# Kernel optimization log

Hardware: AMD Instinct MI355X
Metric: run time of the kernel (lower is better)

Reference implementation:

```python
import jax, jax.numpy as jnp
import numpy as np

E = 16        # num_experts
TOPK = 2      # num_experts_per_tok


def setup_inputs() -> dict:
    key = jax.random.key(0)
    ks = jax.random.split(key, 8)
    B, S, H, I, IS = 4, 2048, 1024, 512, 2048
    std = 0.02
    return {
        "hidden_states": jax.random.normal(ks[0], (B, S, H), jnp.float32),
        "gate_w": jax.random.normal(ks[1], (E, H), jnp.float32) * std,
        "gate_up_proj": jax.random.normal(ks[2], (E, 2 * I, H), jnp.float32) * std,
        "down_proj": jax.random.normal(ks[3], (E, H, I), jnp.float32) * std,
        "shared_gate_proj": jax.random.normal(ks[4], (IS, H), jnp.float32) * std,
        "shared_up_proj": jax.random.normal(ks[5], (IS, H), jnp.float32) * std,
        "shared_down_proj": jax.random.normal(ks[6], (H, IS), jnp.float32) * std,
        "shared_expert_gate_w": jax.random.normal(ks[7], (1, H), jnp.float32) * std,
    }


def _moe(x, gate_w, gate_up_proj, down_proj, sgp, sup, sdp, segw):
    # x: [N, H] flattened tokens
    N = x.shape[0]
    router_logits = x @ gate_w.T                      # [N, E]
    probs = jax.nn.softmax(router_logits, axis=-1)
    routing_weights, selected = jax.lax.top_k(probs, TOPK)   # [N, TOPK]
    routing_weights = routing_weights / routing_weights.sum(-1, keepdims=True)
    # combine weights scattered into dense [N, E] (per-token per-expert gate)
    combine = jnp.zeros((N, E), x.dtype).at[jnp.arange(N)[:, None], selected].add(routing_weights)

    def body(acc, ws):
        gu_w, d_w, cw = ws                            # [2I,H], [H,I], [N]
        gu = x @ gu_w.T                               # [N, 2I]
        g, u = jnp.split(gu, 2, axis=-1)
        h = jax.nn.silu(g) * u                        # [N, I]
        return acc + cw[:, None] * (h @ d_w.T), None

    expert_out, _ = jax.lax.scan(body, jnp.zeros_like(x), (gate_up_proj, down_proj, combine.T))

    # shared expert with sigmoid token gate
    shared_h = jax.nn.silu(x @ sgp.T) * (x @ sup.T)   # [N, IS]
    shared_out = (shared_h @ sdp.T) * jax.nn.sigmoid(x @ segw.T)  # [N, H]
    out = expert_out + shared_out

    # aux (load-balancing) loss
    counts = jnp.sum(jax.nn.one_hot(selected, E, dtype=x.dtype), axis=(0, 1))  # [E]
    frac_tokens = counts / (N * TOPK)
    frac_probs = probs.sum(0) / N
    aux_loss = E * jnp.sum(frac_tokens * frac_probs)
    return out, aux_loss


def reference(hidden_states, gate_w, gate_up_proj, down_proj, shared_gate_proj, shared_up_proj, shared_down_proj, shared_expert_gate_w):
    B, S, H = hidden_states.shape
    out, aux = _moe(hidden_states.reshape(-1, H), gate_w, gate_up_proj, down_proj,
                    shared_gate_proj, shared_up_proj, shared_down_proj, shared_expert_gate_w)
    return out.reshape(B, S, H), aux
```

## Files before the change

### kernel.cpp

```cpp
#include <hip/hip_runtime.h>
#include <hip/hip_bf16.h>
#include <stdint.h>


#define N_TOK 8192
#define HDIM 1024
#define NEXP 16
#define IEXP 512
#define ISH 2048

typedef __bf16 bf16x8 __attribute__((ext_vector_type(8)));
typedef float f32x4 __attribute__((ext_vector_type(4)));

#define OFF_XBF   ((size_t)0)
#define OFF_WSG   ((size_t)16777216)
#define OFF_WSU   ((size_t)20971520)
#define OFF_WSD   ((size_t)25165824)
#define OFF_SH    ((size_t)29360128)
#define OFF_HEXP  ((size_t)62914560)
#define OFF_IDS   ((size_t)79691776)
#define OFF_META  ((size_t)80216064)
#define OFF_SIG   ((size_t)80216320)
#define OFF_LG    ((size_t)80249088)
#define OFF_SLOT  ((size_t)81297664)
#define OFF_TWAB  ((size_t)81363200)

#define WGU_NEW     ((size_t)81428736)
#define NEED_MERGED ((size_t)(WGU_NEW + 33554432))

static __device__ __forceinline__ unsigned short f2bf(float f) {
  unsigned int u = __float_as_uint(f);
  u += 0x7fffu + ((u >> 16) & 1u);
  return (unsigned short)(u >> 16);
}
static __device__ __forceinline__ int pack_bf2(float a, float b) {
  return (int)f2bf(a) | ((int)f2bf(b) << 16);
}
static __device__ __forceinline__ float bf2f(unsigned short u) {
  return __uint_as_float(((unsigned int)u) << 16);
}
static __device__ __forceinline__ void gl_lds16(const void* g, void* l) {
  __builtin_amdgcn_global_load_lds(
      (const __attribute__((address_space(1))) unsigned int*)g,
      (__attribute__((address_space(3))) unsigned int*)l, 16, 0, 0);
}
static __device__ __forceinline__ void barf() {
  asm volatile("" ::: "memory");
  __builtin_amdgcn_s_barrier();
  asm volatile("" ::: "memory");
}

__global__ void cvt_kernel(const float* __restrict__ src,
                           unsigned short* __restrict__ dst, int n4) {
  int i = blockIdx.x * 256 + threadIdx.x;
  if (i >= n4) return;
  float4 v = ((const float4*)src)[i];
  uint2 o;
  o.x = (unsigned)pack_bf2(v.x, v.y);
  o.y = (unsigned)pack_bf2(v.z, v.w);
  ((uint2*)dst)[i] = o;
}

__global__ __launch_bounds__(256) void logits_kernel(
    const float* __restrict__ X, const float* __restrict__ GW,
    const float* __restrict__ SEGW, float* __restrict__ LG,
    unsigned short* __restrict__ XBF) {
  int wid = threadIdx.x >> 6, lane = threadIdx.x & 63;
  int tok = blockIdx.x * 4 + wid;
  const float* xr = X + (size_t)tok * HDIM;
  unsigned short* xw = XBF + (size_t)tok * HDIM;
  float xv[16];
#pragma unroll
  for (int i = 0; i < 16; i++) xv[i] = xr[lane + 64 * i];
#pragma unroll
  for (int i = 0; i < 16; i++) xw[lane + 64 * i] = f2bf(xv[i]);
  float myv = 0.f;
#pragma unroll
  for (int e = 0; e < 17; e++) {
    const float* wr = (e < 16) ? (GW + (size_t)e * HDIM) : SEGW;
    float p = 0.f;
#pragma unroll
    for (int i = 0; i < 16; i++) p += xv[i] * wr[lane + 64 * i];
#pragma unroll
    for (int off = 32; off >= 1; off >>= 1) p += __shfl_xor(p, off, 64);
    if (lane == e) myv = p;
  }
  if (lane < 17) LG[(size_t)tok * 32 + lane] = myv;
}

__global__ __launch_bounds__(256) void route_kernel(
    const float* __restrict__ LG, int* __restrict__ cnt,
    float* __restrict__ pps, int* __restrict__ ids,
    int* __restrict__ slotAB, float* __restrict__ twAB,
    float* __restrict__ sig) {
  __shared__ int lcnt[16];
  __shared__ int lbase[16];
  __shared__ float lps[16];
  int tid = threadIdx.x;
  int tok = blockIdx.x * 256 + tid;
  if (tid < 16) { lcnt[tid] = 0; lps[tid] = 0.f; }
  __syncthreads();
  const float4* row = (const float4*)(LG + (size_t)tok * 32);
  float4 v0 = row[0], v1 = row[1], v2 = row[2], v3 = row[3];
  float g16 = row[4].x;
  float lg[16] = {v0.x, v0.y, v0.z, v0.w, v1.x, v1.y, v1.z, v1.w,
                  v2.x, v2.y, v2.z, v2.w, v3.x, v3.y, v3.z, v3.w};
  float mx = lg[0];
#pragma unroll
  for (int e = 1; e < 16; e++) mx = fmaxf(mx, lg[e]);
  float pr[16], s = 0.f;
#pragma unroll
  for (int e = 0; e < 16; e++) { pr[e] = __expf(lg[e] - mx); s += pr[e]; }
  float inv_s = 1.f / s;
  float p1 = -1.f, p2 = -1.f; int i1 = 0, i2 = 0;
#pragma unroll
  for (int e = 0; e < 16; e++) {
    if (pr[e] > p1) { p2 = p1; i2 = i1; p1 = pr[e]; i1 = e; }
    else if (pr[e] > p2) { p2 = pr[e]; i2 = e; }
  }
  float wsum = p1 + p2;
  int s1 = atomicAdd(&lcnt[i1], 1);
  int s2 = atomicAdd(&lcnt[i2], 1);
#pragma unroll
  for (int e = 0; e < 16; e++) atomicAdd(&lps[e], pr[e] * inv_s);
  sig[tok] = 1.f / (1.f + __expf(-g16));
  __syncthreads();
  if (tid < 16) {
    lbase[tid] = atomicAdd(&cnt[tid], lcnt[tid]);
    atomicAdd(&pps[tid], lps[tid]);
  }
  __syncthreads();
  int sl1 = lbase[i1] + s1, sl2 = lbase[i2] + s2;
  ids[i1 * N_TOK + sl1] = tok;
  ids[i2 * N_TOK + sl2] = tok;
  slotAB[tok * 2]     = (i1 << 14) | sl1;
  slotAB[tok * 2 + 1] = (i2 << 14) | sl2;
  twAB[tok * 2]     = p1 / wsum;
  twAB[tok * 2 + 1] = p2 / wsum;
}

__global__ void offs_aux_kernel(const int* __restrict__ cnt, int* __restrict__ off,
                                const float* __restrict__ probs_sum,
                                float* __restrict__ out_aux) {
  if (threadIdx.x == 0 && blockIdx.x == 0) {
    int run = 0; float aux = 0.f;
    for (int e = 0; e < NEXP; e++) {
      off[e] = run; run += cnt[e];
      aux += ((float)cnt[e] / (float)(N_TOK * 2)) * (probs_sum[e] / (float)N_TOK);
    }
    off[16] = run;
    *out_aux = (float)NEXP * aux;
  }
}

template <int TMODE>
__global__ __launch_bounds__(512, 2) void g8p_kernel(
    const unsigned short* __restrict__ A0,
    const unsigned short* __restrict__ Bg,
    const unsigned short* __restrict__ Bu,
    const unsigned short* __restrict__ Bgu,
    const unsigned short* __restrict__ Bd,
    const int* __restrict__ ids, const int* __restrict__ cnt,
    const int* __restrict__ off,
    unsigned short* __restrict__ Osh,
    unsigned short* __restrict__ Ohex,
    unsigned short* __restrict__ Oeout) {
  constexpr int KD = (TMODE == 2) ? IEXP : HDIM;
  constexpr int NK = KD / 64;
  extern __shared__ unsigned short lds[];

  int rmode, e = 0, bx, by, m0step;
  if constexpr (TMODE == 3) {
    int id = blockIdx.x;
    if (id < 512) { rmode = 0; bx = id & 15; by = id >> 4; m0step = 8192; }
    else {
      int id2 = id - 512;
      rmode = 1; e = id2 >> 5; bx = id2 & 3; by = (id2 >> 2) & 7; m0step = 2048;
    }
  } else if constexpr (TMODE == 0) {
    rmode = 0; bx = blockIdx.x; by = blockIdx.y; m0step = 8192;
  } else if constexpr (TMODE == 1) {
    rmode = 1; e = blockIdx.z; bx = blockIdx.x; by = blockIdx.y;
    m0step = (int)gridDim.y * 256;
  } else {
    rmode = 2; e = blockIdx.z; bx = blockIdx.x; by = blockIdx.y;
    m0step = (int)gridDim.y * 256;
  }

  int ne, base = 0;
  if (rmode == 0) { ne = N_TOK; }
  else { ne = cnt[e]; base = off[e]; }

  const int t = threadIdx.x, lane = t & 63, w = t >> 6;
  const int fr = lane & 15, hi = lane >> 4;
  const int rq = hi * 4;
  const int Rm = (w >> 2) * 64;
  const int wn = (w & 3) * 32;
  const int srow = t >> 3;
  const int sblk = t & 7;
  const int cb = (sblk ^ (srow & 7)) * 8;
  const int s0 = ((0 + hi) ^ (fr & 7)) * 8;
  const int s1 = ((4 + hi) ^ (fr & 7)) * 8;
  const f32x4 z4 = {0.f, 0.f, 0.f, 0.f};

#define STG_A(buf, h, kt)                                                     \
  do {                                                                        \
    gl_lds16(apt[h][0] + (kt) * 64, &lds[(buf)*32768 + (h)*8192 + t * 8]);    \
    gl_lds16(apt[h][1] + (kt) * 64,                                           \
             &lds[(buf)*32768 + (h)*8192 + 4096 + t * 8]);                    \
  } while (0)
#define STG_B(buf, h, kt)                                                     \
  do {                                                                        \
    gl_lds16(bpt[h][0] + (kt) * 64,                                           \
             &lds[(buf)*32768 + 16384 + (h)*8192 + t * 8]);                   \
    gl_lds16(bpt[h][1] + (kt) * 64,                                           \
             &lds[(buf)*32768 + 16384 + (h)*8192 + 4096 + t * 8]);            \
  } while (0)

  for (int m0 = by * 256; m0 < ne; m0 += m0step) {
    const unsigned short* apt[2][2];
    const unsigned short* bpt[2][2];
#pragma unroll
    for (int h = 0; h < 2; h++)
#pragma unroll
      for (int l = 0; l < 2; l++) {
        int r = h * 128 + l * 64 + srow;
        if (rmode == 0) {
          apt[h][l] = A0 + (size_t)(m0 + r) * HDIM + cb;
        } else if (rmode == 1) {
          int slot = m0 + r;
          int arow = (slot < ne) ? ids[e * N_TOK + slot] : 0;
          apt[h][l] = A0 + (size_t)arow * HDIM + cb;
        } else {
          int ra = base + m0 + r;
          if (ra > 16383) ra = 16383;
          apt[h][l] = A0 + (size_t)ra * IEXP + cb;
        }
        if (rmode == 0) {
          int gcol = bx * 128 + ((r >> 5) << 4) + (r & 15);
          const unsigned short* W = (r & 16) ? Bu : Bg;
          bpt[h][l] = W + (size_t)gcol * HDIM + cb;
        } else if (rmode == 1) {
          int wrow = ((r & 16) ? 512 : 0) + bx * 128 + ((r >> 5) << 4) + (r & 15);
          bpt[h][l] = Bgu + ((size_t)e * 1024 + wrow) * HDIM + cb;
        } else {
          int nrow = bx * 256 + r;
          bpt[h][l] = Bd + ((size_t)e * HDIM + nrow) * IEXP + cb;
        }
      }

    f32x4 acc[8][4];
#pragma unroll
    for (int i = 0; i < 8; i++)
#pragma unroll
      for (int j = 0; j < 4; j++) acc[i][j] = z4;

    STG_A(0, 0, 0); STG_B(0, 1, 0); STG_A(0, 1, 0); STG_B(0, 0, 0);
    STG_A(1, 0, 1); STG_B(1, 1, 1);
    asm volatile("s_waitcnt vmcnt(4)" ::: "memory");
    barf();

    for (int kt = 0; kt < NK; ++kt) {
      const int c = kt & 1, nb = c ^ 1;
      const unsigned short* Ab = &lds[c * 32768];
      const unsigned short* Bb = &lds[c * 32768 + 16384];
      bf16x8 a[4][2], b[2][2];

#pragma unroll
      for (int i = 0; i < 4; i++) {
        int ro = (Rm + i * 16 + fr) * 64;
        a[i][0] = *(const bf16x8*)&Ab[ro + s0];
        a[i][1] = *(const bf16x8*)&Ab[ro + s1];
      }
#pragma unroll
      for (int j = 0; j < 2; j++) {
        int ro = (wn + j * 16 + fr) * 64;
        b[j][0] = *(const bf16x8*)&Bb[ro + s0];
        b[j][1] = *(const bf16x8*)&Bb[ro + s1];
      }
      if (kt + 1 < NK) STG_A(nb, 1, kt + 1);
      __builtin_amdgcn_s_setprio(1);
#pragma unroll
      for (int i = 0; i < 4; i++)
#pragma unroll
        for (int j = 0; j < 2; j++) {
          acc[i][j] = __builtin_amdgcn_mfma_f32_16x16x32_bf16(a[i][0], b[j][0], acc[i][j], 0, 0, 0);
          acc[i][j] = __builtin_amdgcn_mfma_f32_16x16x32_bf16(a[i][1], b[j][1], acc[i][j], 0, 0, 0);
        }
      __builtin_amdgcn_s_setprio(0);
      barf();

#pragma unroll
      for (int j = 0; j < 2; j++) {
        int ro = (128 + wn + j * 16 + fr) * 64;
        b[j][0] = *(const bf16x8*)&Bb[ro + s0];
        b[j][1] = *(const bf16x8*)&Bb[ro + s1];
      }
      if (kt + 1 < NK) STG_B(nb, 0, kt + 1);
      __builtin_amdgcn_s_setprio(1);
#pragma unroll
      for (int i = 0; i < 4; i++)
#pragma unroll
        for (int j = 0; j < 2; j++) {
          acc[i][2 + j] = __builtin_amdgcn_mfma_f32_16x16x32_bf16(a[i][0], b[j][0], acc[i][2 + j], 0, 0, 0);
          acc[i][2 + j] = __builtin_amdgcn_mfma_f32_16x16x32_bf16(a[i][1], b[j][1], acc[i][2 + j], 0, 0, 0);
        }
      __builtin_amdgcn_s_setprio(0);
      barf();

#pragma unroll
      for (int i = 0; i < 4; i++) {
        int ro = (128 + Rm + i * 16 + fr) * 64;
        a[i][0] = *(const bf16x8*)&Ab[ro + s0];
        a[i][1] = *(const bf16x8*)&Ab[ro + s1];
      }
      if (kt + 2 < NK) STG_A(c, 0, kt + 2);
      __builtin_amdgcn_s_setprio(1);
#pragma unroll
      for (int i = 0; i < 4; i++)
#pragma unroll
        for (int j = 0; j < 2; j++) {
          acc[4 + i][2 + j] = __builtin_amdgcn_mfma_f32_16x16x32_bf16(a[i][0], b[j][0], acc[4 + i][2 + j], 0, 0, 0);
          acc[4 + i][2 + j] = __builtin_amdgcn_mfma_f32_16x16x32_bf16(a[i][1], b[j][1], acc[4 + i][2 + j], 0, 0, 0);
        }
      __builtin_amdgcn_s_setprio(0);
      barf();

#pragma unroll
      for (int j = 0; j < 2; j++) {
        int ro = (wn + j * 16 + fr) * 64;
        b[j][0] = *(const bf16x8*)&Bb[ro + s0];
        b[j][1] = *(const bf16x8*)&Bb[ro + s1];
      }
      if (kt + 2 < NK) STG_B(c, 1, kt + 2);
      __builtin_amdgcn_s_setprio(1);
#pragma unroll
      for (int i = 0; i < 4; i++)
#pragma unroll
        for (int j = 0; j < 2; j++) {
          acc[4 + i][j] = __builtin_amdgcn_mfma_f32_16x16x32_bf16(a[i][0], b[j][0], acc[4 + i][j], 0, 0, 0);
          acc[4 + i][j] = __builtin_amdgcn_mfma_f32_16x16x32_bf16(a[i][1], b[j][1], acc[4 + i][j], 0, 0, 0);
        }
      __builtin_amdgcn_s_setprio(0);
      if (kt + 2 < NK) asm volatile("s_waitcnt vmcnt(4)" ::: "memory");
      else             asm volatile("s_waitcnt vmcnt(0)" ::: "memory");
      barf();
    }

#pragma unroll
    for (int i = 0; i < 8; i++) {
      int mloc = (i >> 2) * 128 + Rm + (i & 3) * 16 + rq;
      if (rmode == 2) {
#pragma unroll
        for (int j = 0; j < 4; j++) {
          int nn = bx * 256 + (j >> 1) * 128 + wn + (j & 1) * 16 + fr;
#pragma unroll
          for (int r = 0; r < 4; r++) {
            int slot = m0 + mloc + r;
            if (slot < ne)
              Oeout[(size_t)(base + slot) * HDIM + nn] = f2bf(acc[i][j][r]);
          }
        }
      } else {
#pragma unroll
        for (int p = 0; p < 2; p++) {
          int cc = bx * 128 + p * 64 + (w & 3) * 16 + fr;
#pragma unroll
          for (int r = 0; r < 4; r++) {
            int slot = m0 + mloc + r;
            float g = acc[i][2 * p][r], u = acc[i][2 * p + 1][r];
            float hv = g / (1.f + __expf(-g)) * u;
            if (rmode == 0) {
              Osh[(size_t)slot * ISH + cc] = f2bf(hv);
            } else if (slot < ne) {
              Ohex[(size_t)(base + slot) * IEXP + cc] = f2bf(hv);
            }
          }
        }
      }
    }
  }
#undef STG_A
#undef STG_B
}

__global__ __launch_bounds__(256) void shared_gemm2_kernel(
    const unsigned short* __restrict__ H, const unsigned short* __restrict__ Wd,
    const float* __restrict__ sig, float* __restrict__ Out) {
  __shared__ __align__(16) unsigned short As[128 * 32];
  __shared__ __align__(16) unsigned short Bs[128 * 32];
  int m0 = blockIdx.y * 128, n0 = blockIdx.x * 128;
  int t = threadIdx.x, lane = t & 63, w = t >> 6;
  int wm = (w & 1) * 64, wn = (w >> 1) * 64;
  int arow = t >> 2, akb = (t & 3) * 8;
  const unsigned short* apA0 = H + (size_t)(m0 + arow) * ISH + akb;
  const unsigned short* apA1 = H + (size_t)(m0 + 64 + arow) * ISH + akb;
  const unsigned short* apB0 = Wd + (size_t)(n0 + arow) * ISH + akb;
  const unsigned short* apB1 = Wd + (size_t)(n0 + 64 + arow) * ISH + akb;
  f32x4 z = {0.f, 0.f, 0.f, 0.f};
  f32x4 acc[4][4];
#pragma unroll
  for (int i = 0; i < 4; i++)
#pragma unroll
    for (int j = 0; j < 4; j++) acc[i][j] = z;
  for (int k0 = 0; k0 < ISH; k0 += 32) {
    __syncthreads();
    gl_lds16(apA0 + k0, &As[t * 8]);
    gl_lds16(apA1 + k0, &As[2048 + t * 8]);
    gl_lds16(apB0 + k0, &Bs[t * 8]);
    gl_lds16(apB1 + k0, &Bs[2048 + t * 8]);
    __syncthreads();
    int fr = lane & 15, fc = (lane >> 4) * 8;
    bf16x8 af[4], bfr[4];
#pragma unroll
    for (int i = 0; i < 4; i++) {
      af[i] = *(const bf16x8*)&As[(wm + i * 16 + fr) * 32 + fc];
      bfr[i] = *(const bf16x8*)&Bs[(wn + i * 16 + fr) * 32 + fc];
    }
#pragma unroll
    for (int i = 0; i < 4; i++)
#pragma unroll
      for (int j = 0; j < 4; j++)
        acc[i][j] = __builtin_amdgcn_mfma_f32_16x16x32_bf16(af[i], bfr[j], acc[i][j], 0, 0, 0);
  }
  int col = lane & 15, rq = (lane >> 4) * 4;
#pragma unroll
  for (int i = 0; i < 4; i++)
#pragma unroll
    for (int r = 0; r < 4; r++) {
      int mm = m0 + wm + i * 16 + rq + r;
      float sg = sig[mm];
#pragma unroll
      for (int j = 0; j < 4; j++) {
        int nn = n0 + wn + j * 16 + col;
        Out[(size_t)mm * HDIM + nn] = acc[i][j][r] * sg;
      }
    }
}

__global__ __launch_bounds__(256) void combine_kernel(
    const unsigned short* __restrict__ Eout, const int* __restrict__ slotAB,
    const float* __restrict__ twAB, const int* __restrict__ off,
    float* __restrict__ Out) {
  int tok = blockIdx.x, t = threadIdx.x;
  int sa = slotAB[tok * 2], sb = slotAB[tok * 2 + 1];
  float wa = twAB[tok * 2], wb = twAB[tok * 2 + 1];
  int ra = off[sa >> 14] + (sa & 16383);
  int rb = off[sb >> 14] + (sb & 16383);
  const ushort4 a4 = *(const ushort4*)(Eout + (size_t)ra * HDIM + t * 4);
  const ushort4 b4 = *(const ushort4*)(Eout + (size_t)rb * HDIM + t * 4);
  float* po = Out + (size_t)tok * HDIM + t * 4;
  float4 o = *(const float4*)po;
  o.x += wa * bf2f(a4.x) + wb * bf2f(b4.x);
  o.y += wa * bf2f(a4.y) + wb * bf2f(b4.y);
  o.z += wa * bf2f(a4.z) + wb * bf2f(b4.z);
  o.w += wa * bf2f(a4.w) + wb * bf2f(b4.w);
  *(float4*)po = o;
}

extern "C" void kernel_launch(void* const* d_in, const int* in_sizes, int n_in,
                              void* d_out, int out_size, void* d_ws, size_t ws_size,
                              hipStream_t stream) {
  const float* X   = (const float*)d_in[0];
  const float* GW  = (const float*)d_in[1];
  const float* WGU = (const float*)d_in[2];
  const float* WDN = (const float*)d_in[3];
  const float* WSG = (const float*)d_in[4];
  const float* WSU = (const float*)d_in[5];
  const float* WSD = (const float*)d_in[6];
  const float* SEGW = (const float*)d_in[7];
  float* Out = (float*)d_out;
  char* ws = (char*)d_ws;

  unsigned short* xbf  = (unsigned short*)(ws + OFF_XBF);
  unsigned short* wsg  = (unsigned short*)(ws + OFF_WSG);
  unsigned short* wsu  = (unsigned short*)(ws + OFF_WSU);
  unsigned short* wsd  = (unsigned short*)(ws + OFF_WSD);
  unsigned short* sh   = (unsigned short*)(ws + OFF_SH);
  unsigned short* hexp = (unsigned short*)(ws + OFF_HEXP);
  int*   ids  = (int*)(ws + OFF_IDS);
  int*   cnt  = (int*)(ws + OFF_META);
  int*   off  = (int*)(ws + OFF_META + 64);
  float* pps  = (float*)(ws + OFF_META + 144);
  float* sig  = (float*)(ws + OFF_SIG);
  float* lg   = (float*)(ws + OFF_LG);
  int*   slotAB = (int*)(ws + OFF_SLOT);
  float* twAB   = (float*)(ws + OFF_TWAB);

  const bool merged = (ws_size >= NEED_MERGED);
  unsigned short* wgu_bf = (unsigned short*)(ws + (merged ? WGU_NEW : OFF_SH));
  unsigned short* wdn_bf = (unsigned short*)(ws + OFF_XBF);
  unsigned short* eout   = (unsigned short*)(ws + OFF_SH);

  (void)hipFuncSetAttribute((const void*)g8p_kernel<0>,
                            hipFuncAttributeMaxDynamicSharedMemorySize, 131072);
  (void)hipFuncSetAttribute((const void*)g8p_kernel<1>,
                            hipFuncAttributeMaxDynamicSharedMemorySize, 131072);
  (void)hipFuncSetAttribute((const void*)g8p_kernel<2>,
                            hipFuncAttributeMaxDynamicSharedMemorySize, 131072);
  (void)hipFuncSetAttribute((const void*)g8p_kernel<3>,
                            hipFuncAttributeMaxDynamicSharedMemorySize, 131072);

  hipMemsetAsync(ws + OFF_META, 0, 256, stream);

  {
    int n4;
    n4 = (ISH * HDIM) / 4;
    cvt_kernel<<<(n4 + 255) / 256, 256, 0, stream>>>(WSG, wsg, n4);
    cvt_kernel<<<(n4 + 255) / 256, 256, 0, stream>>>(WSU, wsu, n4);
    n4 = (HDIM * ISH) / 4;
    cvt_kernel<<<(n4 + 255) / 256, 256, 0, stream>>>(WSD, wsd, n4);
  }
  if (merged) {
    int n4 = (NEXP * 2 * IEXP * HDIM) / 4;
    cvt_kernel<<<(n4 + 255) / 256, 256, 0, stream>>>(WGU, wgu_bf, n4);
  }

  logits_kernel<<<N_TOK / 4, 256, 0, stream>>>(X, GW, SEGW, lg, xbf);
  route_kernel<<<N_TOK / 256, 256, 0, stream>>>(lg, cnt, pps, ids, slotAB, twAB, sig);
  offs_aux_kernel<<<1, 64, 0, stream>>>(cnt, off, pps, Out + (size_t)N_TOK * HDIM);

  if (merged) {
    g8p_kernel<3><<<dim3(1024), 512, 131072, stream>>>(
        xbf, wsg, wsu, wgu_bf, nullptr, ids, cnt, off, sh, hexp, nullptr);
    shared_gemm2_kernel<<<dim3(HDIM / 128, N_TOK / 128), 256, 0, stream>>>(sh, wsd, sig, Out);
  } else {
    g8p_kernel<0><<<dim3(16, 32), 512, 131072, stream>>>(
        xbf, wsg, wsu, nullptr, nullptr, ids, cnt, off, sh, nullptr, nullptr);
    shared_gemm2_kernel<<<dim3(HDIM / 128, N_TOK / 128), 256, 0, stream>>>(sh, wsd, sig, Out);
    {
      int n4 = (NEXP * 2 * IEXP * HDIM) / 4;
      cvt_kernel<<<(n4 + 255) / 256, 256, 0, stream>>>(WGU, wgu_bf, n4);
    }
    g8p_kernel<1><<<dim3(4, 8, NEXP), 512, 131072, stream>>>(
        xbf, nullptr, nullptr, wgu_bf, nullptr, ids, cnt, off, nullptr, hexp, nullptr);
  }

  {
    int n4 = (NEXP * HDIM * IEXP) / 4;
    cvt_kernel<<<(n4 + 255) / 256, 256, 0, stream>>>(WDN, wdn_bf, n4);
  }
  g8p_kernel<2><<<dim3(HDIM / 256, 8, NEXP), 512, 131072, stream>>>(
      hexp, nullptr, nullptr, nullptr, wdn_bf, ids, cnt, off, nullptr, nullptr, eout);
  combine_kernel<<<N_TOK, 256, 0, stream>>>(eout, slotAB, twAB, off, Out);
}
```

Measured before the change: 509.8 us.

## Fuse weight conversions, fold combine into shared down-proj, add extra barriers

When the workspace is large enough, all five weight tensors are converted to bf16 in one launch, and the expert down-projection now runs before the shared-expert down GEMM. That GEMM's epilogue adds the two routed expert outputs, which removes the separate combine kernel and a read-modify-write of the output. The GEMM main loop also changes its synchronisation: it adds a barrier plus lgkmcnt wait before each MFMA batch and drops the compiler memory fences. The extra barriers may add stall time, and the larger workspace requirement decides which path runs.

Measured after the change: 502.8 us. About the same (-1.4%).

```diff
diff --git a/kernel.cpp b/kernel.cpp
--- a/kernel.cpp
+++ b/kernel.cpp
@@ -25,8 +25,9 @@
 #define OFF_SLOT  ((size_t)81297664)
 #define OFF_TWAB  ((size_t)81363200)
 
-#define WGU_NEW     ((size_t)81428736)
-#define NEED_MERGED ((size_t)(WGU_NEW + 33554432))
+#define WGU_NEW   ((size_t)81428736)
+#define WDN_NEW   ((size_t)(WGU_NEW + 33554432))
+#define NEED_FULL ((size_t)(WDN_NEW + 16777216))
 
 static __device__ __forceinline__ unsigned short f2bf(float f) {
   unsigned int u = __float_as_uint(f);
@@ -43,11 +44,6 @@
   __builtin_amdgcn_global_load_lds(
       (const __attribute__((address_space(1))) unsigned int*)g,
       (__attribute__((address_space(3))) unsigned int*)l, 16, 0, 0);
-}
-static __device__ __forceinline__ void barf() {
-  asm volatile("" ::: "memory");
-  __builtin_amdgcn_s_barrier();
-  asm volatile("" ::: "memory");
 }
 
 __global__ void cvt_kernel(const float* __restrict__ src,
@@ -59,6 +55,32 @@
   o.x = (unsigned)pack_bf2(v.x, v.y);
   o.y = (unsigned)pack_bf2(v.z, v.w);
   ((uint2*)dst)[i] = o;
+}
+
+#define CV_WSG 524288
+#define CV_WSU 1048576
+#define CV_WSD 1572864
+#define CV_WGU 5767168
+#define CV_ALL 7864320
+__global__ void cvt5_kernel(const float* __restrict__ WSG, const float* __restrict__ WSU,
+                            const float* __restrict__ WSD, const float* __restrict__ WGU,
+                            const float* __restrict__ WDN,
+                            unsigned short* __restrict__ wsg, unsigned short* __restrict__ wsu,
+                            unsigned short* __restrict__ wsd, unsigned short* __restrict__ wgu,
+                            unsigned short* __restrict__ wdn) {
+  int i = blockIdx.x * 256 + threadIdx.x;
+  if (i >= CV_ALL) return;
+  const float* src; unsigned short* dst; int k;
+  if (i < CV_WSG)      { src = WSG; dst = wsg; k = i; }
+  else if (i < CV_WSU) { src = WSU; dst = wsu; k = i - CV_WSG; }
+  else if (i < CV_WSD) { src = WSD; dst = wsd; k = i - CV_WSU; }
+  else if (i < CV_WGU) { src = WGU; dst = wgu; k = i - CV_WSD; }
+  else                 { src = WDN; dst = wdn; k = i - CV_WGU; }
+  float4 v = ((const float4*)src)[k];
+  uint2 o;
+  o.x = (unsigned)pack_bf2(v.x, v.y);
+  o.y = (unsigned)pack_bf2(v.z, v.w);
+  ((uint2*)dst)[k] = o;
 }
 
 __global__ __launch_bounds__(256) void logits_kernel(
@@ -258,7 +280,7 @@
     STG_A(0, 0, 0); STG_B(0, 1, 0); STG_A(0, 1, 0); STG_B(0, 0, 0);
     STG_A(1, 0, 1); STG_B(1, 1, 1);
     asm volatile("s_waitcnt vmcnt(4)" ::: "memory");
-    barf();
+    __builtin_amdgcn_s_barrier();
 
     for (int kt = 0; kt < NK; ++kt) {
       const int c = kt & 1, nb = c ^ 1;
@@ -279,6 +301,8 @@
         b[j][1] = *(const bf16x8*)&Bb[ro + s1];
       }
       if (kt + 1 < NK) STG_A(nb, 1, kt + 1);
+      __builtin_amdgcn_s_barrier();
+      asm volatile("s_waitcnt lgkmcnt(0)" ::: "memory");
       __builtin_amdgcn_s_setprio(1);
 #pragma unroll
       for (int i = 0; i < 4; i++)
@@ -288,7 +312,7 @@
           acc[i][j] = __builtin_amdgcn_mfma_f32_16x16x32_bf16(a[i][1], b[j][1], acc[i][j], 0, 0, 0);
         }
       __builtin_amdgcn_s_setprio(0);
-      barf();
+      __builtin_amdgcn_s_barrier();
 
 #pragma unroll
       for (int j = 0; j < 2; j++) {
@@ -297,6 +321,8 @@
         b[j][1] = *(const bf16x8*)&Bb[ro + s1];
       }
       if (kt + 1 < NK) STG_B(nb, 0, kt + 1);
+      __builtin_amdgcn_s_barrier();
+      asm volatile("s_waitcnt lgkmcnt(0)" ::: "memory");
       __builtin_amdgcn_s_setprio(1);
 #pragma unroll
       for (int i = 0; i < 4; i++)
@@ -306,7 +332,7 @@
           acc[i][2 + j] = __builtin_amdgcn_mfma_f32_16x16x32_bf16(a[i][1], b[j][1], acc[i][2 + j], 0, 0, 0);
         }
       __builtin_amdgcn_s_setprio(0);
-      barf();
+      __builtin_amdgcn_s_barrier();
 
 #pragma unroll
       for (int i = 0; i < 4; i++) {
@@ -315,6 +341,8 @@
         a[i][1] = *(const bf16x8*)&Ab[ro + s1];
       }
       if (kt + 2 < NK) STG_A(c, 0, kt + 2);
+      __builtin_amdgcn_s_barrier();
+      asm volatile("s_waitcnt lgkmcnt(0)" ::: "memory");
       __builtin_amdgcn_s_setprio(1);
 #pragma unroll
       for (int i = 0; i < 4; i++)
@@ -324,7 +352,7 @@
           acc[4 + i][2 + j] = __builtin_amdgcn_mfma_f32_16x16x32_bf16(a[i][1], b[j][1], acc[4 + i][2 + j], 0, 0, 0);
         }
       __builtin_amdgcn_s_setprio(0);
-      barf();
+      __builtin_amdgcn_s_barrier();
 
 #pragma unroll
       for (int j = 0; j < 2; j++) {
@@ -333,6 +361,8 @@
         b[j][1] = *(const bf16x8*)&Bb[ro + s1];
       }
       if (kt + 2 < NK) STG_B(c, 1, kt + 2);
+      __builtin_amdgcn_s_barrier();
+      asm volatile("s_waitcnt lgkmcnt(0)" ::: "memory");
       __builtin_amdgcn_s_setprio(1);
 #pragma unroll
       for (int i = 0; i < 4; i++)
@@ -344,7 +374,7 @@
       __builtin_amdgcn_s_setprio(0);
       if (kt + 2 < NK) asm volatile("s_waitcnt vmcnt(4)" ::: "memory");
       else             asm volatile("s_waitcnt vmcnt(0)" ::: "memory");
-      barf();
+      __builtin_amdgcn_s_barrier();
     }
 
 #pragma unroll
@@ -384,9 +414,12 @@
 #undef STG_B
 }
 
-__global__ __launch_bounds__(256) void shared_gemm2_kernel(
+template <int FUSE>
+__global__ __launch_bounds__(256) void sg2c_kernel(
     const unsigned short* __restrict__ H, const unsigned short* __restrict__ Wd,
-    const float* __restrict__ sig, float* __restrict__ Out) {
+    const float* __restrict__ sig, const unsigned short* __restrict__ Eout,
+    const int* __restrict__ slotAB, const float* __restrict__ twAB,
+    const int* __restrict__ off, float* __restrict__ Out) {
   __shared__ __align__(16) unsigned short As[128 * 32];
   __shared__ __align__(16) unsigned short Bs[128 * 32];
   int m0 = blockIdx.y * 128, n0 = blockIdx.x * 128;
@@ -430,10 +463,24 @@
     for (int r = 0; r < 4; r++) {
       int mm = m0 + wm + i * 16 + rq + r;
       float sg = sig[mm];
-#pragma unroll
-      for (int j = 0; j < 4; j++) {
-        int nn = n0 + wn + j * 16 + col;
-        Out[(size_t)mm * HDIM + nn] = acc[i][j][r] * sg;
+      if (FUSE) {
+        int sa = slotAB[mm * 2], sb = slotAB[mm * 2 + 1];
+        float wa = twAB[mm * 2], wb = twAB[mm * 2 + 1];
+        size_t ra = (size_t)(off[sa >> 14] + (sa & 16383)) * HDIM;
+        size_t rb = (size_t)(off[sb >> 14] + (sb & 16383)) * HDIM;
+#pragma unroll
+        for (int j = 0; j < 4; j++) {
+          int nn = n0 + wn + j * 16 + col;
+          float ea = bf2f(Eout[ra + nn]);
+          float eb = bf2f(Eout[rb + nn]);
+          Out[(size_t)mm * HDIM + nn] = acc[i][j][r] * sg + wa * ea + wb * eb;
+        }
+      } else {
+#pragma unroll
+        for (int j = 0; j < 4; j++) {
+          int nn = n0 + wn + j * 16 + col;
+          Out[(size_t)mm * HDIM + nn] = acc[i][j][r] * sg;
+        }
       }
     }
 }
@@ -487,10 +534,7 @@
   int*   slotAB = (int*)(ws + OFF_SLOT);
   float* twAB   = (float*)(ws + OFF_TWAB);
 
-  const bool merged = (ws_size >= NEED_MERGED);
-  unsigned short* wgu_bf = (unsigned short*)(ws + (merged ? WGU_NEW : OFF_SH));
-  unsigned short* wdn_bf = (unsigned short*)(ws + OFF_XBF);
-  unsigned short* eout   = (unsigned short*)(ws + OFF_SH);
+  const bool full = (ws_size >= NEED_FULL);
 
   (void)hipFuncSetAttribute((const void*)g8p_kernel<0>,
                             hipFuncAttributeMaxDynamicSharedMemorySize, 131072);
@@ -503,44 +547,50 @@
 
   hipMemsetAsync(ws + OFF_META, 0, 256, stream);
 
-  {
-    int n4;
-    n4 = (ISH * HDIM) / 4;
+  if (full) {
+    unsigned short* wgu_bf = (unsigned short*)(ws + WGU_NEW);
+    unsigned short* wdn_bf = (unsigned short*)(ws + WDN_NEW);
+    unsigned short* eout   = (unsigned short*)(ws + WGU_NEW);
+
+    cvt5_kernel<<<(CV_ALL + 255) / 256, 256, 0, stream>>>(
+        WSG, WSU, WSD, WGU, WDN, wsg, wsu, wsd, wgu_bf, wdn_bf);
+    logits_kernel<<<N_TOK / 4, 256, 0, stream>>>(X, GW, SEGW, lg, xbf);
+    route_kernel<<<N_TOK / 256, 256, 0, stream>>>(lg, cnt, pps, ids, slotAB, twAB, sig);
+    offs_aux_kernel<<<1, 64, 0, stream>>>(cnt, off, pps, Out + (size_t)N_TOK * HDIM);
+
+    g8p_kernel<3><<<dim3(1024), 512, 131072, stream>>>(
+        xbf, wsg, wsu, wgu_bf, nullptr, ids, cnt, off, sh, hexp, nullptr);
+    g8p_kernel<2><<<dim3(HDIM / 256, 8, NEXP), 512, 131072, stream>>>(
+        hexp, nullptr, nullptr, nullptr, wdn_bf, ids, cnt, off, nullptr, nullptr, eout);
+    sg2c_kernel<1><<<dim3(HDIM / 128, N_TOK / 128), 256, 0, stream>>>(
+        sh, wsd, sig, eout, slotAB, twAB, off, Out);
+  } else {
+    unsigned short* wgu_bf = (unsigned short*)(ws + OFF_SH);
+    unsigned short* wdn_bf = (unsigned short*)(ws + OFF_XBF);
+    unsigned short* eout   = (unsigned short*)(ws + OFF_SH);
+
+    int n4 = (ISH * HDIM) / 4;
     cvt_kernel<<<(n4 + 255) / 256, 256, 0, stream>>>(WSG, wsg, n4);
     cvt_kernel<<<(n4 + 255) / 256, 256, 0, stream>>>(WSU, wsu, n4);
     n4 = (HDIM * ISH) / 4;
     cvt_kernel<<<(n4 + 255) / 256, 256, 0, stream>>>(WSD, wsd, n4);
-  }
-  if (merged) {
-    int n4 = (NEXP * 2 * IEXP * HDIM) / 4;
-    cvt_kernel<<<(n4 + 255) / 256, 256, 0, stream>>>(WGU, wgu_bf, n4);
-  }
-
-  logits_kernel<<<N_TOK / 4, 256, 0, stream>>>(X, GW, SEGW, lg, xbf);
-  route_kernel<<<N_TOK / 256, 256, 0, stream>>>(lg, cnt, pps, ids, slotAB, twAB, sig);
-  offs_aux_kernel<<<1, 64, 0, stream>>>(cnt, off, pps, Out + (size_t)N_TOK * HDIM);
-
-  if (merged) {
-    g8p_kernel<3><<<dim3(1024), 512, 131072, stream>>>(
-        xbf, wsg, wsu, wgu_bf, nullptr, ids, cnt, off, sh, hexp, nullptr);
-    shared_gemm2_kernel<<<dim3(HDIM / 128, N_TOK / 128), 256, 0, stream>>>(sh, wsd, sig, Out);
-  } else {
+
+    logits_kernel<<<N_TOK / 4, 256, 0, stream>>>(X, GW, SEGW, lg, xbf);
+    route_kernel<<<N_TOK / 256, 256, 0, stream>>>(lg, cnt, pps, ids, slotAB, twAB, sig);
+    offs_aux_kernel<<<1, 64, 0, stream>>>(cnt, off, pps, Out + (size_t)N_TOK * HDIM);
+
     g8p_kernel<0><<<dim3(16, 32), 512, 131072, stream>>>(
         xbf, wsg, wsu, nullptr, nullptr, ids, cnt, off, sh, nullptr, nullptr);
-    shared_gemm2_kernel<<<dim3(HDIM / 128, N_TOK / 128), 256, 0, stream>>>(sh, wsd, sig, Out);
-    {
-      int n4 = (NEXP * 2 * IEXP * HDIM) / 4;
-      cvt_kernel<<<(n4 + 255) / 256, 256, 0, stream>>>(WGU, wgu_bf, n4);
-    }
+    sg2c_kernel<0><<<dim3(HDIM / 128, N_TOK / 128), 256, 0, stream>>>(
+        sh, wsd, sig, nullptr, slotAB, twAB, off, Out);
+    n4 = (NEXP * 2 * IEXP * HDIM) / 4;
+    cvt_kernel<<<(n4 + 255) / 256, 256, 0, stream>>>(WGU, wgu_bf, n4);
     g8p_kernel<1><<<dim3(4, 8, NEXP), 512, 131072, stream>>>(
         xbf, nullptr, nullptr, wgu_bf, nullptr, ids, cnt, off, nullptr, hexp, nullptr);
-  }
-
-  {
-    int n4 = (NEXP * HDIM * IEXP) / 4;
+    n4 = (NEXP * HDIM * IEXP) / 4;
     cvt_kernel<<<(n4 + 255) / 256, 256, 0, stream>>>(WDN, wdn_bf, n4);
-  }
-  g8p_kernel<2><<<dim3(HDIM / 256, 8, NEXP), 512, 131072, stream>>>(
-      hexp, nullptr, nullptr, nullptr, wdn_bf, ids, cnt, off, nullptr, nullptr, eout);
-  combine_kernel<<<N_TOK, 256, 0, stream>>>(eout, slotAB, twAB, off, Out);
-}
+    g8p_kernel<2><<<dim3(HDIM / 256, 8, NEXP), 512, 131072, stream>>>(
+        hexp, nullptr, nullptr, nullptr, wdn_bf, ids, cnt, off, nullptr, nullptr, eout);
+    combine_kernel<<<N_TOK, 256, 0, stream>>>(eout, slotAB, twAB, off, Out);
+  }
+}
```
